# Performance work log

Hardware: AMD Instinct MI355X
Metric: run time of the kernel (lower is better)

## Reference

```python
import jax, jax.numpy as jnp
import numpy as np

B, S, F, H, C, L = 256, 128, 128, 512, 64, 16


def setup_inputs() -> dict:
    key = jax.random.key(0)
    ks = jax.random.split(key, 16)
    stdv = 1.0 / np.sqrt(H)
    u = lambda k, shape, s=stdv: jax.random.uniform(k, shape, jnp.float32, -s, s)
    W_ih = u(ks[0], (F, 4 * H))
    b_ih = u(ks[1], (4 * H,)).at[H:2 * H].set(1.0)  # forget-gate bias init = 1
    W_hh = u(ks[2], (H, 4 * H))
    b_hh = u(ks[3], (4 * H,)).at[H:2 * H].set(1.0)
    cg_w1 = u(ks[4], (C, H))
    cg_b1 = u(ks[5], (H,))
    cg_w2 = u(ks[6], (H, 3 * H))
    cg_b2 = jnp.ones((3 * H,), jnp.float32)  # context_gate[-2].bias.fill_(1.0)
    mu_w = u(ks[7], (H, L))
    mu_b = u(ks[8], (L,))
    lv_w = u(ks[9], (H, L))
    lv_b = u(ks[10], (L,))
    dec_w1 = u(ks[11], (L, H))
    dec_b1 = u(ks[12], (H,))
    dec_w2 = u(ks[13], (H, F))
    dec_b2 = u(ks[14], (F,))
    kx, kc, ke = jax.random.split(ks[15], 3)
    return dict(
        x=jax.random.normal(kx, (B, S, F), jnp.float32),
        context=jax.random.normal(kc, (B, C), jnp.float32),
        eps=jax.random.normal(ke, (B, L), jnp.float32),
        W_ih=W_ih, b_ih=b_ih, W_hh=W_hh, b_hh=b_hh,
        cg_w1=cg_w1, cg_b1=cg_b1, cg_w2=cg_w2, cg_b2=cg_b2,
        mu_w=mu_w, mu_b=mu_b, lv_w=lv_w, lv_b=lv_b,
        dec_w1=dec_w1, dec_b1=dec_b1, dec_w2=dec_w2, dec_b2=dec_b2,
    )


def reference(x, context, eps, W_ih, b_ih, W_hh, b_hh, cg_w1, cg_b1, cg_w2, cg_b2,
              mu_w, mu_b, lv_w, lv_b, dec_w1, dec_b1, dec_w2, dec_b2):
    Bsz, Slen, _ = x.shape
    Hd = W_hh.shape[0]
    # context is static across time -> context-gate computed once (same math as
    # recomputing identically at each step)
    ctx = jax.nn.sigmoid(jax.nn.relu(context @ cg_w1 + cg_b1) @ cg_w2 + cg_b2)  # [B, 3H]
    ci, cf, co = jnp.split(ctx, 3, axis=1)
    # precompute input projections for all timesteps: [S, B, 4H]
    xg = jnp.einsum('bsf,fk->sbk', x, W_ih) + b_ih

    def step(carry, xg_t):
        h, c = carry
        gates = xg_t + h @ W_hh + b_hh
        i, f, g, o = jnp.split(gates, 4, axis=1)
        i = jax.nn.sigmoid(i) * ci
        f = jax.nn.sigmoid(f) * cf
        g = jnp.tanh(g)
        o = jax.nn.sigmoid(o) * co
        c_next = f * c + i * g
        h_next = o * jnp.tanh(c_next)
        return (h_next, c_next), None

    h0 = jnp.zeros((Bsz, Hd), x.dtype)
    (h, _), _ = jax.lax.scan(step, (h0, h0), xg)

    mu = h @ mu_w + mu_b
    log_var = h @ lv_w + lv_b
    z = mu + eps * jnp.exp(0.5 * log_var)  # reparameterize
    recon_x = jax.nn.relu(z @ dec_w1 + dec_b1) @ dec_w2 + dec_b2
    return recon_x, mu, log_var
```

## Files before the change

kernel.cpp:

```cpp
#include <hip/hip_runtime.h>
#include <cstdint>
#include <cstddef>

#define B_ 256
#define S_ 128
#define F_ 128
#define H_ 512
#define C_ 64
#define L_ 16

typedef __attribute__((ext_vector_type(8))) short short8;
typedef __attribute__((ext_vector_type(4))) float f4;
typedef __attribute__((ext_vector_type(4))) unsigned int u4;

__device__ __forceinline__ unsigned short f2bf(float f) {
  union { float f; unsigned u; } v; v.f = f;
  unsigned r = v.u + 0x7fffu + ((v.u >> 16) & 1u);
  return (unsigned short)(r >> 16);
}
__device__ __forceinline__ float sigmoid_(float x) { return 1.0f / (1.0f + __expf(-x)); }
__device__ __forceinline__ float tanh_(float x) {
  x = fminf(15.f, fmaxf(-15.f, x));
  float e = __expf(2.f * x);
  return (e - 1.f) / (e + 1.f);
}

__global__ void prep_kernel(const float* __restrict__ x, const float* __restrict__ W_hh,
                            const float* __restrict__ W_ih, const float* __restrict__ b_ih,
                            const float* __restrict__ b_hh, const float* __restrict__ context,
                            const float* __restrict__ w1, const float* __restrict__ b1,
                            const float* __restrict__ w2, const float* __restrict__ b2,
                            unsigned short* __restrict__ xfr, unsigned short* __restrict__ Wpk,
                            unsigned short* __restrict__ Wipk, float* __restrict__ bc,
                            float* __restrict__ ctxg) {
  int bid = blockIdx.x, tid = threadIdx.x;
  if (bid < 2048) {
    int o8 = bid * 256 + tid;
    int m = o8 & 15, kb = (o8 >> 4) & 15, Rg = (o8 >> 8) & 15, s = o8 >> 12;
    int b = Rg * 16 + m;
    const float* src = x + (b * S_ + s) * F_ + kb * 8;
    unsigned short* dst = xfr + o8 * 8;
#pragma unroll
    for (int j = 0; j < 8; j++) dst[j] = f2bf(src[j]);
    return;
  }
  if (bid < 2696) {
    int t = (bid - 2048) * 256 + tid;
    if (t < 131072) {
      int lane = t & 63, row = t >> 6;
      int kit = row & 15, gh = row >> 4;
      int g = gh & 3, ht = gh >> 2;
      int k0 = kit * 32 + ((lane >> 4) << 3);
      int col = g * 512 + ht * 16 + (lane & 15);
#pragma unroll
      for (int j = 0; j < 8; j++)
        Wpk[t * 8 + j] = f2bf(W_hh[(k0 + j) * 2048 + col]);
    } else if (t < 131072 + 32768) {
      int t2 = t - 131072;
      int lane = t2 & 63, row = t2 >> 6;
      int kit = row & 3, gh = row >> 2;
      int g = gh & 3, ht = gh >> 2;
      int k0 = kit * 32 + ((lane >> 4) << 3);
      int col = g * 512 + ht * 16 + (lane & 15);
#pragma unroll
      for (int j = 0; j < 8; j++)
        Wipk[t2 * 8 + j] = f2bf(W_ih[(k0 + j) * 2048 + col]);
    } else if (t < 131072 + 32768 + 2048) {
      int i = t - 131072 - 32768;
      bc[i] = b_ih[i] + b_hh[i];
    }
    return;
  }
  {
    __shared__ float hr[4 * H_];
    __shared__ float cc[4 * C_];
    int r0 = (bid - 2696) * 4, t = tid;
    if (t < 4 * C_) cc[t] = context[r0 * C_ + t];
    __syncthreads();
    for (int rj = t; rj < 4 * H_; rj += 256) {
      int r = rj >> 9, j = rj & 511;
      float acc = b1[j];
#pragma unroll 8
      for (int k = 0; k < C_; k++) acc = fmaf(cc[r * C_ + k], w1[k * H_ + j], acc);
      hr[rj] = fmaxf(acc, 0.f);
    }
    __syncthreads();
    float acc[4][6];
#pragma unroll
    for (int r = 0; r < 4; r++)
#pragma unroll
      for (int i = 0; i < 6; i++) acc[r][i] = 0.f;
    for (int k = 0; k < H_; k++) {
      float w[6];
#pragma unroll
      for (int i = 0; i < 6; i++) w[i] = w2[k * 1536 + t + i * 256];
#pragma unroll
      for (int r = 0; r < 4; r++) {
        float hv = hr[r * H_ + k];
#pragma unroll
        for (int i = 0; i < 6; i++) acc[r][i] = fmaf(hv, w[i], acc[r][i]);
      }
    }
#pragma unroll
    for (int r = 0; r < 4; r++)
#pragma unroll
      for (int i = 0; i < 6; i++) {
        int col = t + i * 256;
        ctxg[(r0 + r) * 1536 + col] = sigmoid_(acc[r][i] + b2[col]);
      }
  }
}

__global__ void __launch_bounds__(256) lstm_kernel(
    const unsigned short* __restrict__ xfr, const unsigned short* __restrict__ Wpk,
    const unsigned short* __restrict__ Wipk, const float* __restrict__ bc,
    const float* __restrict__ ctxg, float* __restrict__ hfinal,
    unsigned short* __restrict__ hb0, unsigned short* __restrict__ hb1,
    unsigned int* __restrict__ flags) {
  __shared__ __align__(16) unsigned short lds_h[16384];
  __shared__ __align__(16) unsigned short lds_x[4096];
  __shared__ float lds_g[128 * 17];

  int tid = threadIdx.x, lane = tid & 63, wid = tid >> 6;
  int bt = blockIdx.x >> 5, ht = blockIdx.x & 31;

  short8 wf[16], wfi[4];
  {
    const short8* wp = (const short8*)Wpk + (ht * 4 + wid) * 16 * 64 + lane;
#pragma unroll
    for (int kit = 0; kit < 16; kit++) wf[kit] = wp[kit * 64];
    const short8* wip = (const short8*)Wipk + (ht * 4 + wid) * 4 * 64 + lane;
#pragma unroll
    for (int kit = 0; kit < 4; kit++) wfi[kit] = wip[kit * 64];
  }

  int bl = tid >> 3, jl0 = (tid & 7) * 2;
  int bglob = bt * 32 + bl;
  int j0 = ht * 16 + jl0;
  float cst[2] = {0.f, 0.f};
  float ci_[2], cf_[2], co_[2], bi_[2], bf_[2], bg_[2], bo_[2];
#pragma unroll
  for (int p = 0; p < 2; p++) {
    int j = j0 + p;
    ci_[p] = ctxg[bglob * 1536 + j];
    cf_[p] = ctxg[bglob * 1536 + 512 + j];
    co_[p] = ctxg[bglob * 1536 + 1024 + j];
    bi_[p] = bc[j]; bf_[p] = bc[512 + j]; bg_[p] = bc[1024 + j]; bo_[p] = bc[1536 + j];
  }
  int hoff2 = (((bt * 2 + (bl >> 4)) * 64 + ht * 2 + (jl0 >> 3)) * 128
               + (bl & 15) * 8 + (jl0 & 7)) >> 1;

  const unsigned int* fb = flags + bt * 32;
  unsigned int* myflag = flags + bt * 32 + ht;

#pragma unroll
  for (int i = 0; i < 2; i++) {
    int c = wid * 2 + i, R = c >> 2, kit = c & 3;
    u4 d = *(const u4*)(xfr + (size_t)((bt * 2 + R) * 16 + kit * 4) * 128 + lane * 8);
    *(u4*)(lds_x + (R * 4 + kit) * 512 + lane * 8) = d;
  }
  __syncthreads();

  for (int t = 0; t < S_; t++) {
    const unsigned short* hread = (t & 1) ? hb1 : hb0;
    unsigned short* hwrite = (t & 1) ? hb0 : hb1;

    f4 acc0a = {0.f, 0.f, 0.f, 0.f}, acc1a = {0.f, 0.f, 0.f, 0.f};
    f4 acc0b = {0.f, 0.f, 0.f, 0.f}, acc1b = {0.f, 0.f, 0.f, 0.f};

#pragma unroll
    for (int kit = 0; kit < 4; kit++) {
      short8 a0 = *(const short8*)(lds_x + kit * 512 + lane * 8);
      short8 a1 = *(const short8*)(lds_x + 2048 + kit * 512 + lane * 8);
      if (kit & 1) {
        acc0b = __builtin_amdgcn_mfma_f32_16x16x32_bf16(a0, wfi[kit], acc0b, 0, 0, 0);
        acc1b = __builtin_amdgcn_mfma_f32_16x16x32_bf16(a1, wfi[kit], acc1b, 0, 0, 0);
      } else {
        acc0a = __builtin_amdgcn_mfma_f32_16x16x32_bf16(a0, wfi[kit], acc0a, 0, 0, 0);
        acc1a = __builtin_amdgcn_mfma_f32_16x16x32_bf16(a1, wfi[kit], acc1a, 0, 0, 0);
      }
    }

    if (t > 0) {
      const unsigned int* fp = fb + (lane & 31);
      unsigned tgt = (unsigned)t;
      for (;;) {
        unsigned v = __hip_atomic_load(fp, __ATOMIC_RELAXED, __HIP_MEMORY_SCOPE_AGENT);
        if (__all(v >= tgt)) break;
      }

      u4 tmp[8];
#pragma unroll
      for (int i = 0; i < 8; i++) {
        int c = wid * 8 + i, R = c >> 4, kit = c & 15;
        const unsigned int* src = (const unsigned int*)hread
            + (bt * 2 + R) * 4096 + kit * 256 + lane * 4;
        asm volatile("global_load_dwordx4 %0, %1, off sc0 sc1"
                     : "=v"(tmp[i]) : "v"(src) : "memory");
      }

      asm volatile("s_waitcnt vmcnt(0)"
                   : "+v"(tmp[0]), "+v"(tmp[1]), "+v"(tmp[2]), "+v"(tmp[3]),
                     "+v"(tmp[4]), "+v"(tmp[5]), "+v"(tmp[6]), "+v"(tmp[7])
                   :: "memory");
#pragma unroll
      for (int i = 0; i < 8; i++) {
        int c = wid * 8 + i, R = c >> 4, kit = c & 15;
        *(u4*)(lds_h + R * 8192 + kit * 512 + lane * 8) = tmp[i];
      }
      __syncthreads();

#pragma unroll
      for (int kit = 0; kit < 16; kit++) {
        short8 a0 = *(const short8*)(lds_h + kit * 512 + lane * 8);
        short8 a1 = *(const short8*)(lds_h + 8192 + kit * 512 + lane * 8);
        if (kit & 1) {
          acc0b = __builtin_amdgcn_mfma_f32_16x16x32_bf16(a0, wf[kit], acc0b, 0, 0, 0);
          acc1b = __builtin_amdgcn_mfma_f32_16x16x32_bf16(a1, wf[kit], acc1b, 0, 0, 0);
        } else {
          acc0a = __builtin_amdgcn_mfma_f32_16x16x32_bf16(a0, wf[kit], acc0a, 0, 0, 0);
          acc1a = __builtin_amdgcn_mfma_f32_16x16x32_bf16(a1, wf[kit], acc1a, 0, 0, 0);
        }
      }
    }

    {
      f4 s0, s1;
#pragma unroll
      for (int r = 0; r < 4; r++) { s0[r] = acc0a[r] + acc0b[r]; s1[r] = acc1a[r] + acc1b[r]; }
      int q = lane >> 4, n = lane & 15;
#pragma unroll
      for (int r = 0; r < 4; r++) {
        lds_g[(wid * 32 + q * 4 + r) * 17 + n] = s0[r];
        lds_g[(wid * 32 + 16 + q * 4 + r) * 17 + n] = s1[r];
      }
    }
    __syncthreads();

    {
      float hv[2];
#pragma unroll
      for (int p = 0; p < 2; p++) {
        int jl = jl0 + p;
        float gi = lds_g[(0 * 32 + bl) * 17 + jl] + bi_[p];
        float gf = lds_g[(1 * 32 + bl) * 17 + jl] + bf_[p];
        float gg = lds_g[(2 * 32 + bl) * 17 + jl] + bg_[p];
        float go = lds_g[(3 * 32 + bl) * 17 + jl] + bo_[p];
        float iv = ci_[p] * sigmoid_(gi);
        float fv = cf_[p] * sigmoid_(gf);
        float ov = co_[p] * sigmoid_(go);
        float gv = tanh_(gg);
        float c = fv * cst[p] + iv * gv;
        cst[p] = c;
        hv[p] = ov * tanh_(c);
      }
      unsigned int packed = (unsigned)f2bf(hv[0]) | ((unsigned)f2bf(hv[1]) << 16);
      unsigned int* dst = (unsigned int*)hwrite + hoff2;
      asm volatile("global_store_dword %0, %1, off sc0 sc1"
                   :: "v"(dst), "v"(packed) : "memory");
      if (t == S_ - 1) {
        hfinal[bglob * H_ + j0] = hv[0];
        hfinal[bglob * H_ + j0 + 1] = hv[1];
      }
    }

    if (t < S_ - 1) {
      asm volatile("s_waitcnt vmcnt(0)" ::: "memory");
      __syncthreads();
      if (tid == 0) {
        unsigned val = (unsigned)(t + 1);
        asm volatile("global_store_dword %0, %1, off sc0 sc1"
                     :: "v"(myflag), "v"(val) : "memory");
      }
#pragma unroll
      for (int i = 0; i < 2; i++) {
        int c = wid * 2 + i, R = c >> 2, kit = c & 3;
        u4 d = *(const u4*)(xfr + (size_t)((((t + 1) * 16) + bt * 2 + R) * 16 + kit * 4) * 128 + lane * 8);
        *(u4*)(lds_x + (R * 4 + kit) * 512 + lane * 8) = d;
      }
    }
    __syncthreads();
  }
}

__global__ void post_kernel(const float* __restrict__ hfinal, const float* __restrict__ eps,
                            const float* __restrict__ mu_w, const float* __restrict__ mu_b,
                            const float* __restrict__ lv_w, const float* __restrict__ lv_b,
                            const float* __restrict__ dw1, const float* __restrict__ db1,
                            const float* __restrict__ dw2, const float* __restrict__ db2,
                            float* __restrict__ out) {
  __shared__ float sh[H_], sh1[H_], smu[L_], slv[L_], sz[L_];
  int b = blockIdx.x, t = threadIdx.x;
  for (int i = t; i < H_; i += 256) sh[i] = hfinal[b * H_ + i];
  __syncthreads();
  {
    int o = t >> 3, sub = t & 7, l = o & 15;
    const float* w = (o < 16) ? mu_w : lv_w;
    float acc = 0.f;
    int k0 = sub * 64;
#pragma unroll 8
    for (int k = k0; k < k0 + 64; k++) acc = fmaf(sh[k], w[k * L_ + l], acc);
#pragma unroll
    for (int d = 4; d >= 1; d >>= 1) acc += __shfl_down(acc, d, 8);
    if (sub == 0) {
      if (o < 16) { float v = acc + mu_b[l]; smu[l] = v; out[32768 + b * 16 + l] = v; }
      else        { float v = acc + lv_b[l]; slv[l] = v; out[36864 + b * 16 + l] = v; }
    }
  }
  __syncthreads();
  if (t < L_) sz[t] = smu[t] + eps[b * L_ + t] * __expf(0.5f * slv[t]);
  __syncthreads();
  for (int j = t; j < H_; j += 256) {
    float acc = db1[j];
#pragma unroll
    for (int l = 0; l < L_; l++) acc = fmaf(sz[l], dw1[l * H_ + j], acc);
    sh1[j] = fmaxf(acc, 0.f);
  }
  __syncthreads();
  if (t < F_) {
    float acc = db2[t];
    for (int k = 0; k < H_; k++) acc = fmaf(sh1[k], dw2[k * F_ + t], acc);
    out[b * F_ + t] = acc;
  }
}

extern "C" void kernel_launch(void* const* d_in, const int* in_sizes, int n_in,
                              void* d_out, int out_size, void* d_ws, size_t ws_size,
                              hipStream_t stream) {
  const float* x      = (const float*)d_in[0];
  const float* ctxin  = (const float*)d_in[1];
  const float* eps    = (const float*)d_in[2];
  const float* W_ih   = (const float*)d_in[3];
  const float* b_ih   = (const float*)d_in[4];
  const float* W_hh   = (const float*)d_in[5];
  const float* b_hh   = (const float*)d_in[6];
  const float* cg_w1  = (const float*)d_in[7];
  const float* cg_b1  = (const float*)d_in[8];
  const float* cg_w2  = (const float*)d_in[9];
  const float* cg_b2  = (const float*)d_in[10];
  const float* mu_w   = (const float*)d_in[11];
  const float* mu_b   = (const float*)d_in[12];
  const float* lv_w   = (const float*)d_in[13];
  const float* lv_b   = (const float*)d_in[14];
  const float* dec_w1 = (const float*)d_in[15];
  const float* dec_b1 = (const float*)d_in[16];
  const float* dec_w2 = (const float*)d_in[17];
  const float* dec_b2 = (const float*)d_in[18];
  float* out = (float*)d_out;

  char* ws = (char*)d_ws;
  size_t off = 0;
  auto alloc = [&](size_t bytes) { char* p = ws + off; off = (off + bytes + 255) & ~(size_t)255; return p; };

  unsigned int* flags = (unsigned int*)alloc(8 * 32 * 4);
  size_t zero_bytes = off;
  unsigned short* hb0 = (unsigned short*)alloc(B_ * H_ * 2);
  unsigned short* hb1 = (unsigned short*)alloc(B_ * H_ * 2);
  unsigned short* xfr  = (unsigned short*)alloc((size_t)B_ * S_ * F_ * 2);
  unsigned short* Wpk  = (unsigned short*)alloc((size_t)H_ * 2048 * 2);
  unsigned short* Wipk = (unsigned short*)alloc((size_t)F_ * 2048 * 2);
  float* bc    = (float*)alloc(2048 * 4);
  float* ctxg  = (float*)alloc((size_t)B_ * 1536 * 4);
  float* hfin  = (float*)alloc((size_t)B_ * H_ * 4);
  (void)ws_size; (void)in_sizes; (void)n_in; (void)out_size;

  hipMemsetAsync(d_ws, 0, zero_bytes, stream);

  prep_kernel<<<2760, 256, 0, stream>>>(x, W_hh, W_ih, b_ih, b_hh, ctxin,
                                        cg_w1, cg_b1, cg_w2, cg_b2,
                                        xfr, Wpk, Wipk, bc, ctxg);
  lstm_kernel<<<256, 256, 0, stream>>>(xfr, Wpk, Wipk, bc, ctxg, hfin, hb0, hb1,
                                       flags);
  post_kernel<<<256, 256, 0, stream>>>(hfin, eps, mu_w, mu_b, lv_w, lv_b,
                                       dec_w1, dec_b1, dec_w2, dec_b2, out);
}
```

Before: 610.7 us.

## Use per-step unique h buffers, per-wave flags, and overlap input MFMA with loads

Allocates one hidden-state buffer per timestep when workspace permits, so reads can use sc0-only loads instead of bypassing caches, since stale lines cannot alias. Replaces the block-wide syncthreads before flag publish with per-wave flags, and pollers check 128 flags. The input-projection MFMAs are moved after issuing h loads to hide load latency. Adds workspace usage of 16MB and relies on ws_size being large enough; the per-wave flag scheme must preserve store visibility ordering.

```diff
diff --git a/kernel.cpp b/kernel.cpp
--- a/kernel.cpp
+++ b/kernel.cpp
@@ -115,14 +115,15 @@
     const unsigned short* __restrict__ xfr, const unsigned short* __restrict__ Wpk,
     const unsigned short* __restrict__ Wipk, const float* __restrict__ bc,
     const float* __restrict__ ctxg, float* __restrict__ hfinal,
-    unsigned short* __restrict__ hb0, unsigned short* __restrict__ hb1,
-    unsigned int* __restrict__ flags) {
+    unsigned short* __restrict__ hbase, unsigned int* __restrict__ flags,
+    int hmask) {
   __shared__ __align__(16) unsigned short lds_h[16384];
   __shared__ __align__(16) unsigned short lds_x[4096];
   __shared__ float lds_g[128 * 17];
 
   int tid = threadIdx.x, lane = tid & 63, wid = tid >> 6;
   int bt = blockIdx.x >> 5, ht = blockIdx.x & 31;
+  const bool cached = (hmask == 127);
 
   short8 wf[16], wfi[4];
   {
@@ -150,8 +151,9 @@
   int hoff2 = (((bt * 2 + (bl >> 4)) * 64 + ht * 2 + (jl0 >> 3)) * 128
                + (bl & 15) * 8 + (jl0 & 7)) >> 1;
 
-  const unsigned int* fb = flags + bt * 32;
-  unsigned int* myflag = flags + bt * 32 + ht;
+  unsigned int* myflag = flags + bt * 128 + ht * 4 + wid;
+  const unsigned int* fp0 = flags + bt * 128 + lane;
+  const unsigned int* fp1 = fp0 + 64;
 
 #pragma unroll
   for (int i = 0; i < 2; i++) {
@@ -162,30 +164,18 @@
   __syncthreads();
 
   for (int t = 0; t < S_; t++) {
-    const unsigned short* hread = (t & 1) ? hb1 : hb0;
-    unsigned short* hwrite = (t & 1) ? hb0 : hb1;
+    const unsigned short* hread = hbase + (size_t)((t - 1) & hmask) * (B_ * H_);
+    unsigned short* hwrite = (unsigned short*)hbase + (size_t)(t & hmask) * (B_ * H_);
 
     f4 acc0a = {0.f, 0.f, 0.f, 0.f}, acc1a = {0.f, 0.f, 0.f, 0.f};
     f4 acc0b = {0.f, 0.f, 0.f, 0.f}, acc1b = {0.f, 0.f, 0.f, 0.f};
 
-#pragma unroll
-    for (int kit = 0; kit < 4; kit++) {
-      short8 a0 = *(const short8*)(lds_x + kit * 512 + lane * 8);
-      short8 a1 = *(const short8*)(lds_x + 2048 + kit * 512 + lane * 8);
-      if (kit & 1) {
-        acc0b = __builtin_amdgcn_mfma_f32_16x16x32_bf16(a0, wfi[kit], acc0b, 0, 0, 0);
-        acc1b = __builtin_amdgcn_mfma_f32_16x16x32_bf16(a1, wfi[kit], acc1b, 0, 0, 0);
-      } else {
-        acc0a = __builtin_amdgcn_mfma_f32_16x16x32_bf16(a0, wfi[kit], acc0a, 0, 0, 0);
-        acc1a = __builtin_amdgcn_mfma_f32_16x16x32_bf16(a1, wfi[kit], acc1a, 0, 0, 0);
-      }
-    }
-
     if (t > 0) {
-      const unsigned int* fp = fb + (lane & 31);
       unsigned tgt = (unsigned)t;
       for (;;) {
-        unsigned v = __hip_atomic_load(fp, __ATOMIC_RELAXED, __HIP_MEMORY_SCOPE_AGENT);
+        unsigned a = __hip_atomic_load(fp0, __ATOMIC_RELAXED, __HIP_MEMORY_SCOPE_AGENT);
+        unsigned b = __hip_atomic_load(fp1, __ATOMIC_RELAXED, __HIP_MEMORY_SCOPE_AGENT);
+        unsigned v = (a < b) ? a : b;
         if (__all(v >= tgt)) break;
       }
 
@@ -195,8 +185,25 @@
         int c = wid * 8 + i, R = c >> 4, kit = c & 15;
         const unsigned int* src = (const unsigned int*)hread
             + (bt * 2 + R) * 4096 + kit * 256 + lane * 4;
-        asm volatile("global_load_dwordx4 %0, %1, off sc0 sc1"
-                     : "=v"(tmp[i]) : "v"(src) : "memory");
+        if (cached)
+          asm volatile("global_load_dwordx4 %0, %1, off sc0"
+                       : "=v"(tmp[i]) : "v"(src) : "memory");
+        else
+          asm volatile("global_load_dwordx4 %0, %1, off sc0 sc1"
+                       : "=v"(tmp[i]) : "v"(src) : "memory");
+      }
+
+#pragma unroll
+      for (int kit = 0; kit < 4; kit++) {
+        short8 a0 = *(const short8*)(lds_x + kit * 512 + lane * 8);
+        short8 a1 = *(const short8*)(lds_x + 2048 + kit * 512 + lane * 8);
+        if (kit & 1) {
+          acc0b = __builtin_amdgcn_mfma_f32_16x16x32_bf16(a0, wfi[kit], acc0b, 0, 0, 0);
+          acc1b = __builtin_amdgcn_mfma_f32_16x16x32_bf16(a1, wfi[kit], acc1b, 0, 0, 0);
+        } else {
+          acc0a = __builtin_amdgcn_mfma_f32_16x16x32_bf16(a0, wfi[kit], acc0a, 0, 0, 0);
+          acc1a = __builtin_amdgcn_mfma_f32_16x16x32_bf16(a1, wfi[kit], acc1a, 0, 0, 0);
+        }
       }
 
       asm volatile("s_waitcnt vmcnt(0)"
@@ -221,6 +228,14 @@
           acc0a = __builtin_amdgcn_mfma_f32_16x16x32_bf16(a0, wf[kit], acc0a, 0, 0, 0);
           acc1a = __builtin_amdgcn_mfma_f32_16x16x32_bf16(a1, wf[kit], acc1a, 0, 0, 0);
         }
+      }
+    } else {
+#pragma unroll
+      for (int kit = 0; kit < 4; kit++) {
+        short8 a0 = *(const short8*)(lds_x + kit * 512 + lane * 8);
+        short8 a1 = *(const short8*)(lds_x + 2048 + kit * 512 + lane * 8);
+        acc0a = __builtin_amdgcn_mfma_f32_16x16x32_bf16(a0, wfi[kit], acc0a, 0, 0, 0);
+        acc1a = __builtin_amdgcn_mfma_f32_16x16x32_bf16(a1, wfi[kit], acc1a, 0, 0, 0);
       }
     }
 
@@ -266,8 +281,7 @@
 
     if (t < S_ - 1) {
       asm volatile("s_waitcnt vmcnt(0)" ::: "memory");
-      __syncthreads();
-      if (tid == 0) {
+      if (lane == 0) {
         unsigned val = (unsigned)(t + 1);
         asm volatile("global_store_dword %0, %1, off sc0 sc1"
                      :: "v"(myflag), "v"(val) : "memory");
@@ -352,25 +366,33 @@
   size_t off = 0;
   auto alloc = [&](size_t bytes) { char* p = ws + off; off = (off + bytes + 255) & ~(size_t)255; return p; };
 
-  unsigned int* flags = (unsigned int*)alloc(8 * 32 * 4);
+  unsigned int* flags = (unsigned int*)alloc(8 * 128 * 4);
   size_t zero_bytes = off;
-  unsigned short* hb0 = (unsigned short*)alloc(B_ * H_ * 2);
-  unsigned short* hb1 = (unsigned short*)alloc(B_ * H_ * 2);
   unsigned short* xfr  = (unsigned short*)alloc((size_t)B_ * S_ * F_ * 2);
   unsigned short* Wpk  = (unsigned short*)alloc((size_t)H_ * 2048 * 2);
   unsigned short* Wipk = (unsigned short*)alloc((size_t)F_ * 2048 * 2);
   float* bc    = (float*)alloc(2048 * 4);
   float* ctxg  = (float*)alloc((size_t)B_ * 1536 * 4);
   float* hfin  = (float*)alloc((size_t)B_ * H_ * 4);
-  (void)ws_size; (void)in_sizes; (void)n_in; (void)out_size;
+  size_t h_unique_bytes = (size_t)S_ * B_ * H_ * 2;
+  int hmask;
+  unsigned short* hbase;
+  if (ws_size >= off + h_unique_bytes) {
+    hbase = (unsigned short*)alloc(h_unique_bytes);
+    hmask = 127;
+  } else {
+    hbase = (unsigned short*)alloc((size_t)2 * B_ * H_ * 2);
+    hmask = 1;
+  }
+  (void)in_sizes; (void)n_in; (void)out_size;
 
   hipMemsetAsync(d_ws, 0, zero_bytes, stream);
 
   prep_kernel<<<2760, 256, 0, stream>>>(x, W_hh, W_ih, b_ih, b_hh, ctxin,
                                         cg_w1, cg_b1, cg_w2, cg_b2,
                                         xfr, Wpk, Wipk, bc, ctxg);
-  lstm_kernel<<<256, 256, 0, stream>>>(xfr, Wpk, Wipk, bc, ctxg, hfin, hb0, hb1,
-                                       flags);
+  lstm_kernel<<<256, 256, 0, stream>>>(xfr, Wpk, Wipk, bc, ctxg, hfin,
+                                       hbase, flags, hmask);
   post_kernel<<<256, 256, 0, stream>>>(hfin, eps, mu_w, mu_b, lv_w, lv_b,
                                        dec_w1, dec_b1, dec_w2, dec_b2, out);
 }
```

Measured after the change: 588.7 us. -3.6%, faster.
